# Kernel optimization log

Hardware: AMD Instinct MI355X
Metric: run time of the kernel (lower is better)

The kernel has to match this reference:

```python
import jax, jax.numpy as jnp
import numpy as np

NUM_HEADS = 16


def setup_inputs() -> dict:
    key = jax.random.key(0)
    ks = jax.random.split(key, 5)
    b, s, d = 2, 2048, 1024
    std = (2.0 / (d + d)) ** 0.5
    x = jax.random.normal(ks[0], (b, s, d), dtype=jnp.float32)
    Wq = jax.random.normal(ks[1], (d, d), dtype=jnp.float32) * std
    Wk = jax.random.normal(ks[2], (d, d), dtype=jnp.float32) * std
    Wv = jax.random.normal(ks[3], (d, d), dtype=jnp.float32) * std
    Wo = jax.random.normal(ks[4], (d, d), dtype=jnp.float32) * std
    return {"x": x, "Wq": Wq, "Wk": Wk, "Wv": Wv, "Wo": Wo}


def reference(x, Wq, Wk, Wv, Wo):
    b, s, d = x.shape
    h = NUM_HEADS
    dk = d // h
    # projections: bias-free x @ W (W is [in, out])
    def split_heads(t):
        return t.reshape(b, s, h, dk).transpose(0, 2, 1, 3)  # b h s dk
    q = split_heads(x @ Wq)
    k = split_heads(x @ Wk)
    v = split_heads(x @ Wv)
    scale = 1.0 / jnp.sqrt(jnp.asarray(dk, dtype=x.dtype))
    scores = jnp.einsum('bhqd,bhkd->bhqk', q, k) * scale  # b h s s
    causal = jnp.tril(jnp.ones((s, s), dtype=bool))
    scores = jnp.where(causal, scores, -jnp.inf)
    probs = jax.nn.softmax(scores, axis=-1)
    out = jnp.einsum('bhqk,bhkd->bhqd', probs, v)
    out = out.transpose(0, 2, 1, 3).reshape(b, s, d)  # b s (h dk)
    return out @ Wo
```

## Files before the change

### kernel.cpp

```cpp
#include <hip/hip_runtime.h>

typedef unsigned short u16;
typedef unsigned int   u32;

using bf16x8 = __attribute__((ext_vector_type(8))) __bf16;
using bf16x4 = __attribute__((ext_vector_type(4))) __bf16;
using f32x4  = __attribute__((ext_vector_type(4))) float;
using s16x4  = __attribute__((ext_vector_type(4))) short;

#define NH    16
#define DKH   64
#define SEQ   2048
#define BAT   2
#define DMOD  1024

#define QSCALE 0.18033688011112042f

__device__ __forceinline__ u16 f2bf(float f) {
  union { float f; u32 u; } v; v.f = f;
  u32 r = v.u + 0x7fffu + ((v.u >> 16) & 1u);
  return (u16)(r >> 16);
}

__device__ __forceinline__ u32 pack2bf(float a, float b) {
  union { float f; u32 u; } x, y; x.f = a; y.f = b;
  u32 ua = x.u + 0x7fffu + ((x.u >> 16) & 1u);
  u32 ub = y.u + 0x7fffu + ((y.u >> 16) & 1u);
  return __builtin_amdgcn_perm(ub, ua, 0x07060302u);
}

__device__ __forceinline__ s16x4 pk4bf(float a, float b, float c, float d) {
  union { bf16x4 bv; s16x4 sv; } u;
  u.bv[0] = (__bf16)a; u.bv[1] = (__bf16)b; u.bv[2] = (__bf16)c; u.bv[3] = (__bf16)d;
  return u.sv;
}

#if __has_builtin(__builtin_amdgcn_exp2f)
#define EXP2(x) __builtin_amdgcn_exp2f(x)
#else
#define EXP2(x) exp2f(x)
#endif

#if __has_builtin(__builtin_amdgcn_mfma_f32_16x16x16bf16_1k)
__device__ __forceinline__ f32x4 mfma16(s16x4 a, s16x4 b, f32x4 c) {
  return __builtin_amdgcn_mfma_f32_16x16x16bf16_1k(a, b, c, 0, 0, 0);
}
#else
__device__ __forceinline__ f32x4 mfma16(s16x4 a, s16x4 b, f32x4 c) {
  f32x4 d;
  asm volatile("v_mfma_f32_16x16x16_bf16 %0, %1, %2, %3\n\ts_nop 7\n\ts_nop 7"
               : "=v"(d) : "v"(a), "v"(b), "v"(c));
  return d;
}
#endif

__global__ __launch_bounds__(256) void transpose_all(const float* __restrict__ Wq,
                                                     const float* __restrict__ Wk,
                                                     const float* __restrict__ Wv,
                                                     const float* __restrict__ Wo,
                                                     u16* __restrict__ Wt) {
  __shared__ u16 t[32][33];
  const float* W = blockIdx.z == 0 ? Wq : blockIdx.z == 1 ? Wk : blockIdx.z == 2 ? Wv : Wo;
  u16* o = Wt + (size_t)blockIdx.z * DMOD * DMOD;
  int bx = blockIdx.x * 32, by = blockIdx.y * 32;
  int x = threadIdx.x, y = threadIdx.y;
  #pragma unroll
  for (int i = 0; i < 32; i += 8)
    t[y + i][x] = f2bf(W[(size_t)(by + y + i) * DMOD + bx + x]);
  __syncthreads();
  #pragma unroll
  for (int i = 0; i < 32; i += 8)
    o[(size_t)(bx + y + i) * DMOD + by + x] = t[x][y + i];
}

__global__ __launch_bounds__(256) void convert_x(const float* __restrict__ x,
                                                 u16* __restrict__ xb) {
  size_t i = ((size_t)blockIdx.x * 256 + threadIdx.x) * 8;
  float4 f0 = *(const float4*)(x + i);
  float4 f1 = *(const float4*)(x + i + 4);
  uint4 o;
  o.x = pack2bf(f0.x, f0.y); o.y = pack2bf(f0.z, f0.w);
  o.z = pack2bf(f1.x, f1.y); o.w = pack2bf(f1.z, f1.w);
  *(uint4*)(xb + i) = o;
}

__global__ __launch_bounds__(256, 3) void gemm_qkv(const u16* __restrict__ A,
                                                   const u16* __restrict__ Bt,
                                                   u16* __restrict__ Qo,
                                                   u16* __restrict__ Ko,
                                                   u16* __restrict__ Vo) {
  __shared__ __align__(16) u16 As[128 * 40];
  __shared__ __align__(16) u16 Bs[128 * 40];
  const int tid  = threadIdx.x;
  const int lane = tid & 63, wv = tid >> 6;
  const int wm   = wv >> 1, wn = wv & 1;
  const int lrow = lane & 15, quad = lane >> 4;
  const int tileM = blockIdx.x * 128, tileN = blockIdx.y * 128;
  const int r0 = tid >> 2, c0 = (tid & 3) * 8;
  const int r1 = r0 + 64;

  const f32x4 fz = {0.f, 0.f, 0.f, 0.f};
  f32x4 acc[4][4];
  #pragma unroll
  for (int i = 0; i < 4; ++i)
    #pragma unroll
    for (int j = 0; j < 4; ++j) acc[i][j] = fz;

  uint4 a0 = *(const uint4*)(&A [(size_t)(tileM + r0) * DMOD + c0]);
  uint4 a1 = *(const uint4*)(&A [(size_t)(tileM + r1) * DMOD + c0]);
  uint4 b0 = *(const uint4*)(&Bt[(size_t)(tileN + r0) * DMOD + c0]);
  uint4 b1 = *(const uint4*)(&Bt[(size_t)(tileN + r1) * DMOD + c0]);

  for (int kt = 0; kt < DMOD; kt += 32) {
    __syncthreads();
    *(uint4*)(&As[r0 * 40 + c0]) = a0;
    *(uint4*)(&As[r1 * 40 + c0]) = a1;
    *(uint4*)(&Bs[r0 * 40 + c0]) = b0;
    *(uint4*)(&Bs[r1 * 40 + c0]) = b1;
    if (kt + 32 < DMOD) {
      a0 = *(const uint4*)(&A [(size_t)(tileM + r0) * DMOD + kt + 32 + c0]);
      a1 = *(const uint4*)(&A [(size_t)(tileM + r1) * DMOD + kt + 32 + c0]);
      b0 = *(const uint4*)(&Bt[(size_t)(tileN + r0) * DMOD + kt + 32 + c0]);
      b1 = *(const uint4*)(&Bt[(size_t)(tileN + r1) * DMOD + kt + 32 + c0]);
    }
    __syncthreads();
    bf16x8 af[4], bfr[4];
    #pragma unroll
    for (int mt = 0; mt < 4; ++mt)
      af[mt] = *(const bf16x8*)(&As[(wm * 64 + mt * 16 + lrow) * 40 + quad * 8]);
    #pragma unroll
    for (int nt = 0; nt < 4; ++nt)
      bfr[nt] = *(const bf16x8*)(&Bs[(wn * 64 + nt * 16 + lrow) * 40 + quad * 8]);
    #pragma unroll
    for (int mt = 0; mt < 4; ++mt)
      #pragma unroll
      for (int nt = 0; nt < 4; ++nt)
        acc[mt][nt] = __builtin_amdgcn_mfma_f32_16x16x32_bf16(af[mt], bfr[nt],
                                                              acc[mt][nt], 0, 0, 0);
  }

  #pragma unroll
  for (int mt = 0; mt < 4; ++mt) {
    #pragma unroll
    for (int nt = 0; nt < 4; ++nt) {
      int gm0 = tileM + wm * 64 + mt * 16 + quad * 4;
      int gn  = tileN + wn * 64 + nt * 16 + lrow;
      int which = gn >> 10, col = gn & 1023;
      int bb = gm0 >> 11, srw0 = gm0 & (SEQ - 1);
      int hh = col >> 6, dki = col & (DKH - 1);
      size_t bhi = (size_t)(bb * NH + hh);
      if (which == 0) {
        #pragma unroll
        for (int r = 0; r < 4; ++r)
          Qo[(bhi * SEQ + srw0 + r) * DKH + dki] = f2bf(acc[mt][nt][r] * QSCALE);
      } else if (which == 1) {
        #pragma unroll
        for (int r = 0; r < 4; ++r)
          Ko[(bhi * SEQ + srw0 + r) * DKH + dki] = f2bf(acc[mt][nt][r]);
      } else {
        uint2 pk;
        pk.x = pack2bf(acc[mt][nt][0], acc[mt][nt][1]);
        pk.y = pack2bf(acc[mt][nt][2], acc[mt][nt][3]);
        *(uint2*)(&Vo[(((bhi * (SEQ / 4)) + (srw0 >> 2)) * DKH + dki) * 4]) = pk;
      }
    }
  }
}

__global__ __launch_bounds__(256, 3) void gemm_out(const u16* __restrict__ A,
                                                   const u16* __restrict__ Bt,
                                                   float* __restrict__ Co) {
  __shared__ __align__(16) u16 As[128 * 40];
  __shared__ __align__(16) u16 Bs[64 * 40];
  const int tid  = threadIdx.x;
  const int lane = tid & 63, wv = tid >> 6;
  const int wm   = wv & 1, wn = wv >> 1;
  const int lrow = lane & 15, quad = lane >> 4;
  const int tileM = blockIdx.x * 128, tileN = blockIdx.y * 64;
  const int r0 = tid >> 2, c0 = (tid & 3) * 8;
  const int r1 = r0 + 64;

  const f32x4 fz = {0.f, 0.f, 0.f, 0.f};
  f32x4 acc[4][2];
  #pragma unroll
  for (int i = 0; i < 4; ++i) { acc[i][0] = fz; acc[i][1] = fz; }

  uint4 a0 = *(const uint4*)(&A [(size_t)(tileM + r0) * DMOD + c0]);
  uint4 a1 = *(const uint4*)(&A [(size_t)(tileM + r1) * DMOD + c0]);
  uint4 b0 = *(const uint4*)(&Bt[(size_t)(tileN + (r0 & 63)) * DMOD + c0]);

  for (int kt = 0; kt < DMOD; kt += 32) {
    __syncthreads();
    *(uint4*)(&As[r0 * 40 + c0]) = a0;
    *(uint4*)(&As[r1 * 40 + c0]) = a1;
    if (r0 < 64) *(uint4*)(&Bs[r0 * 40 + c0]) = b0;
    if (kt + 32 < DMOD) {
      a0 = *(const uint4*)(&A [(size_t)(tileM + r0) * DMOD + kt + 32 + c0]);
      a1 = *(const uint4*)(&A [(size_t)(tileM + r1) * DMOD + kt + 32 + c0]);
      b0 = *(const uint4*)(&Bt[(size_t)(tileN + (r0 & 63)) * DMOD + kt + 32 + c0]);
    }
    __syncthreads();
    bf16x8 af[4], bfr[2];
    #pragma unroll
    for (int mt = 0; mt < 4; ++mt)
      af[mt] = *(const bf16x8*)(&As[(wm * 64 + mt * 16 + lrow) * 40 + quad * 8]);
    #pragma unroll
    for (int nt = 0; nt < 2; ++nt)
      bfr[nt] = *(const bf16x8*)(&Bs[(wn * 32 + nt * 16 + lrow) * 40 + quad * 8]);
    #pragma unroll
    for (int mt = 0; mt < 4; ++mt)
      #pragma unroll
      for (int nt = 0; nt < 2; ++nt)
        acc[mt][nt] = __builtin_amdgcn_mfma_f32_16x16x32_bf16(af[mt], bfr[nt],
                                                              acc[mt][nt], 0, 0, 0);
  }

  #pragma unroll
  for (int mt = 0; mt < 4; ++mt)
    #pragma unroll
    for (int nt = 0; nt < 2; ++nt)
      #pragma unroll
      for (int r = 0; r < 4; ++r) {
        int gm = tileM + wm * 64 + mt * 16 + quad * 4 + r;
        int gn = tileN + wn * 32 + nt * 16 + lrow;
        Co[(size_t)gm * DMOD + gn] = acc[mt][nt][r];
      }
}

#define KP 72
#define VP 132
#define OP 68

__global__ __launch_bounds__(128, 2) void attn_k(const u16* __restrict__ Q,
                                                 const u16* __restrict__ Kg,
                                                 const u16* __restrict__ Vg,
                                                 u16* __restrict__ Og) {
  __shared__ __align__(16) u16 Ks[128 * KP];
  __shared__ __align__(16) u16 Vs[64 * VP];

  const int tid  = threadIdx.x;
  const int lane = tid & 63, w = tid >> 6;
  const int lrow = lane & 15, quad = lane >> 4;
  const int bh = blockIdx.x;
  const int t  = blockIdx.y;
  const int qb = (t < 16) ? t : 47 - t;
  const int b = bh >> 4, h = bh & 15;
  const int jmax = qb >> 1;
  const int qoff = qb & 1;

  const u16* Qbh = Q  + (size_t)bh * SEQ * DKH;
  const u16* Kbh = Kg + (size_t)bh * SEQ * DKH;
  const u16* Vbh = Vg + (size_t)bh * SEQ * DKH;

  bf16x8 bq[2][2];
  #pragma unroll
  for (int s = 0; s < 2; ++s)
    #pragma unroll
    for (int kk = 0; kk < 2; ++kk)
      bq[s][kk] = *(const bf16x8*)(&Qbh[(size_t)(qb * 64 + (2 * w + s) * 16 + lrow) * DKH
                                        + kk * 32 + quad * 8]);

  uint4 kreg[8], vreg[8];
  #pragma unroll
  for (int k = 0; k < 8; ++k) {
    int ci = k * 128 + tid;
    kreg[k] = *(const uint4*)(&Kbh[(size_t)(ci >> 3) * DKH + (ci & 7) * 8]);
    vreg[k] = *(const uint4*)(&Vbh[(size_t)(ci >> 5) * 256 + (ci & 31) * 8]);
  }

  const f32x4 fz = {0.f, 0.f, 0.f, 0.f};
  f32x4 oacc[2][4];
  #pragma unroll
  for (int s = 0; s < 2; ++s)
    #pragma unroll
    for (int d = 0; d < 4; ++d) oacc[s][d] = fz;
  float lsum[2] = {0.f, 0.f};

  for (int j = 0; j <= jmax; ++j) {
    if (j) __syncthreads();

    #pragma unroll
    for (int k = 0; k < 8; ++k) {
      int ci = k * 128 + tid;
      *(uint4*)(&Ks[(ci >> 3) * KP + (ci & 7) * 8]) = kreg[k];
      int sq = ci >> 5, dkp = ci & 31;
      union { uint4 q; uint2 d[2]; } vv; vv.q = vreg[k];
      *(uint2*)(&Vs[(2 * dkp)     * VP + 4 * sq]) = vv.d[0];
      *(uint2*)(&Vs[(2 * dkp + 1) * VP + 4 * sq]) = vv.d[1];
    }

    if (j < jmax) {
      const int jn = j + 1;
      #pragma unroll
      for (int k = 0; k < 8; ++k) {
        int ci = k * 128 + tid;
        kreg[k] = *(const uint4*)(&Kbh[(size_t)(jn * 128 + (ci >> 3)) * DKH + (ci & 7) * 8]);
        vreg[k] = *(const uint4*)(&Vbh[(size_t)(jn * 32 + (ci >> 5)) * 256 + (ci & 31) * 8]);
      }
    }

    __syncthreads();

    if (j < jmax) {
      f32x4 sacc[2][8];
      #pragma unroll
      for (int s = 0; s < 2; ++s)
        #pragma unroll
        for (int m = 0; m < 8; ++m) sacc[s][m] = fz;
      #pragma unroll
      for (int kk = 0; kk < 2; ++kk)
        #pragma unroll
        for (int m = 0; m < 8; ++m) {
          bf16x8 ak = *(const bf16x8*)(&Ks[(m * 16 + lrow) * KP + kk * 32 + quad * 8]);
          sacc[0][m] = __builtin_amdgcn_mfma_f32_16x16x32_bf16(ak, bq[0][kk], sacc[0][m], 0, 0, 0);
          sacc[1][m] = __builtin_amdgcn_mfma_f32_16x16x32_bf16(ak, bq[1][kk], sacc[1][m], 0, 0, 0);
        }
      #pragma unroll
      for (int m = 0; m < 8; ++m) {
        float p00 = EXP2(sacc[0][m][0]), p01 = EXP2(sacc[0][m][1]);
        float p02 = EXP2(sacc[0][m][2]), p03 = EXP2(sacc[0][m][3]);
        float p10 = EXP2(sacc[1][m][0]), p11 = EXP2(sacc[1][m][1]);
        float p12 = EXP2(sacc[1][m][2]), p13 = EXP2(sacc[1][m][3]);
        lsum[0] += (p00 + p01) + (p02 + p03);
        lsum[1] += (p10 + p11) + (p12 + p13);
        s16x4 pk0 = pk4bf(p00, p01, p02, p03);
        s16x4 pk1 = pk4bf(p10, p11, p12, p13);
        #pragma unroll
        for (int d = 0; d < 4; ++d) {
          s16x4 av = *(const s16x4*)(&Vs[(d * 16 + lrow) * VP + m * 16 + quad * 4]);
          oacc[0][d] = mfma16(av, pk0, oacc[0][d]);
          oacc[1][d] = mfma16(av, pk1, oacc[1][d]);
        }
      }
    } else {
      #pragma unroll
      for (int s = 0; s < 2; ++s) {
        const int L = qoff * 4 + 2 * w + s;
        for (int m = 0; m < L; ++m) {
          f32x4 sv = fz;
          #pragma unroll
          for (int kk = 0; kk < 2; ++kk) {
            bf16x8 ak = *(const bf16x8*)(&Ks[(m * 16 + lrow) * KP + kk * 32 + quad * 8]);
            sv = __builtin_amdgcn_mfma_f32_16x16x32_bf16(ak, bq[s][kk], sv, 0, 0, 0);
          }
          float p0 = EXP2(sv[0]), p1 = EXP2(sv[1]), p2 = EXP2(sv[2]), p3 = EXP2(sv[3]);
          lsum[s] += (p0 + p1) + (p2 + p3);
          s16x4 pk = pk4bf(p0, p1, p2, p3);
          #pragma unroll
          for (int d = 0; d < 4; ++d) {
            s16x4 av = *(const s16x4*)(&Vs[(d * 16 + lrow) * VP + m * 16 + quad * 4]);
            oacc[s][d] = mfma16(av, pk, oacc[s][d]);
          }
        }
        {
          f32x4 sv = fz;
          #pragma unroll
          for (int kk = 0; kk < 2; ++kk) {
            bf16x8 ak = *(const bf16x8*)(&Ks[(L * 16 + lrow) * KP + kk * 32 + quad * 8]);
            sv = __builtin_amdgcn_mfma_f32_16x16x32_bf16(ak, bq[s][kk], sv, 0, 0, 0);
          }
          float p[4];
          #pragma unroll
          for (int r = 0; r < 4; ++r)
            p[r] = (quad * 4 + r > lrow) ? 0.f : EXP2(sv[r]);
          lsum[s] += (p[0] + p[1]) + (p[2] + p[3]);
          s16x4 pk = pk4bf(p[0], p[1], p[2], p[3]);
          #pragma unroll
          for (int d = 0; d < 4; ++d) {
            s16x4 av = *(const s16x4*)(&Vs[(d * 16 + lrow) * VP + L * 16 + quad * 4]);
            oacc[s][d] = mfma16(av, pk, oacc[s][d]);
          }
        }
      }
    }
  }

  float inv[2];
  #pragma unroll
  for (int s = 0; s < 2; ++s) {
    float ls = lsum[s];
    ls += __shfl_xor(ls, 16, 64);
    ls += __shfl_xor(ls, 32, 64);
    inv[s] = 1.f / ls;
  }

  __syncthreads();
  u16* Osr = Ks;
  #pragma unroll
  for (int s = 0; s < 2; ++s) {
    int row = (2 * w + s) * 16 + lrow;
    #pragma unroll
    for (int d = 0; d < 4; ++d) {
      uint2 pkk;
      pkk.x = pack2bf(oacc[s][d][0] * inv[s], oacc[s][d][1] * inv[s]);
      pkk.y = pack2bf(oacc[s][d][2] * inv[s], oacc[s][d][3] * inv[s]);
      *(uint2*)(&Osr[row * OP + d * 16 + quad * 4]) = pkk;
    }
  }
  __syncthreads();
  #pragma unroll
  for (int k = 0; k < 4; ++k) {
    int c = k * 128 + tid;
    int row = c >> 3, ch = c & 7;
    uint4 v = *(const uint4*)(&Osr[row * OP + ch * 8]);
    *(uint4*)(&Og[(size_t)(b * SEQ + qb * 64 + row) * DMOD + h * DKH + ch * 8]) = v;
  }
}

extern "C" void kernel_launch(void* const* d_in, const int* in_sizes, int n_in,
                              void* d_out, int out_size, void* d_ws, size_t ws_size,
                              hipStream_t stream) {
  const float* x  = (const float*)d_in[0];
  const float* Wq = (const float*)d_in[1];
  const float* Wk = (const float*)d_in[2];
  const float* Wv = (const float*)d_in[3];
  const float* Wo = (const float*)d_in[4];

  u16* ws = (u16*)d_ws;
  const size_t WSZ = (size_t)DMOD * DMOD;
  const size_t TSZ = (size_t)BAT * NH * SEQ * DKH;
  u16* Wt  = ws;
  u16* Wto = Wt + 3 * WSZ;
  u16* xb  = Wt + 4 * WSZ;
  u16* Qb  = xb + TSZ;
  u16* Kb  = Qb + TSZ;
  u16* Vb  = Kb + TSZ;
  u16* Ob  = xb;

  transpose_all<<<dim3(32, 32, 4), dim3(32, 8), 0, stream>>>(Wq, Wk, Wv, Wo, Wt);
  convert_x<<<dim3(2048), 256, 0, stream>>>(x, xb);

  gemm_qkv<<<dim3(32, 24), 256, 0, stream>>>(xb, Wt, Qb, Kb, Vb);

  attn_k<<<dim3(32, 32), 128, 0, stream>>>(Qb, Kb, Vb, Ob);

  gemm_out<<<dim3(32, 16), 256, 0, stream>>>(Ob, Wto, (float*)d_out);
}
```

Baseline: 195.1 us.

## Use direct global-to-LDS loads in GEMMs and double-buffer larger attention tiles

Result: faster. 181.1 us (-7.2%).

```diff
diff --git a/kernel.cpp b/kernel.cpp
--- a/kernel.cpp
+++ b/kernel.cpp
@@ -53,6 +53,12 @@
   return d;
 }
 #endif
+
+typedef const __attribute__((address_space(1))) u32 glb_u32;
+typedef __attribute__((address_space(3))) u32 lds_u32;
+__device__ __forceinline__ void gload16(const u16* g, u16* l) {
+  __builtin_amdgcn_global_load_lds((glb_u32*)(const void*)g, (lds_u32*)(void*)l, 16, 0, 0);
+}
 
 __global__ __launch_bounds__(256) void transpose_all(const float* __restrict__ Wq,
                                                      const float* __restrict__ Wk,
@@ -89,15 +95,13 @@
                                                    u16* __restrict__ Qo,
                                                    u16* __restrict__ Ko,
                                                    u16* __restrict__ Vo) {
-  __shared__ __align__(16) u16 As[128 * 40];
-  __shared__ __align__(16) u16 Bs[128 * 40];
+  __shared__ __align__(16) u16 As[128 * 32];
+  __shared__ __align__(16) u16 Bs[128 * 32];
   const int tid  = threadIdx.x;
   const int lane = tid & 63, wv = tid >> 6;
   const int wm   = wv >> 1, wn = wv & 1;
   const int lrow = lane & 15, quad = lane >> 4;
   const int tileM = blockIdx.x * 128, tileN = blockIdx.y * 128;
-  const int r0 = tid >> 2, c0 = (tid & 3) * 8;
-  const int r1 = r0 + 64;
 
   const f32x4 fz = {0.f, 0.f, 0.f, 0.f};
   f32x4 acc[4][4];
@@ -106,31 +110,23 @@
     #pragma unroll
     for (int j = 0; j < 4; ++j) acc[i][j] = fz;
 
-  uint4 a0 = *(const uint4*)(&A [(size_t)(tileM + r0) * DMOD + c0]);
-  uint4 a1 = *(const uint4*)(&A [(size_t)(tileM + r1) * DMOD + c0]);
-  uint4 b0 = *(const uint4*)(&Bt[(size_t)(tileN + r0) * DMOD + c0]);
-  uint4 b1 = *(const uint4*)(&Bt[(size_t)(tileN + r1) * DMOD + c0]);
-
   for (int kt = 0; kt < DMOD; kt += 32) {
+    if (kt) __syncthreads();
+    #pragma unroll
+    for (int i = 0; i < 2; ++i) {
+      int idx = i * 256 + tid;
+      gload16(&A [(size_t)(tileM + (idx >> 2)) * DMOD + kt + (idx & 3) * 8], &As[idx * 8]);
+      gload16(&Bt[(size_t)(tileN + (idx >> 2)) * DMOD + kt + (idx & 3) * 8], &Bs[idx * 8]);
+    }
     __syncthreads();
-    *(uint4*)(&As[r0 * 40 + c0]) = a0;
-    *(uint4*)(&As[r1 * 40 + c0]) = a1;
-    *(uint4*)(&Bs[r0 * 40 + c0]) = b0;
-    *(uint4*)(&Bs[r1 * 40 + c0]) = b1;
-    if (kt + 32 < DMOD) {
-      a0 = *(const uint4*)(&A [(size_t)(tileM + r0) * DMOD + kt + 32 + c0]);
-      a1 = *(const uint4*)(&A [(size_t)(tileM + r1) * DMOD + kt + 32 + c0]);
-      b0 = *(const uint4*)(&Bt[(size_t)(tileN + r0) * DMOD + kt + 32 + c0]);
-      b1 = *(const uint4*)(&Bt[(size_t)(tileN + r1) * DMOD + kt + 32 + c0]);
-    }
-    __syncthreads();
+
     bf16x8 af[4], bfr[4];
     #pragma unroll
     for (int mt = 0; mt < 4; ++mt)
-      af[mt] = *(const bf16x8*)(&As[(wm * 64 + mt * 16 + lrow) * 40 + quad * 8]);
+      af[mt] = *(const bf16x8*)(&As[(wm * 64 + mt * 16 + lrow) * 32 + quad * 8]);
     #pragma unroll
     for (int nt = 0; nt < 4; ++nt)
-      bfr[nt] = *(const bf16x8*)(&Bs[(wn * 64 + nt * 16 + lrow) * 40 + quad * 8]);
+      bfr[nt] = *(const bf16x8*)(&Bs[(wn * 64 + nt * 16 + lrow) * 32 + quad * 8]);
     #pragma unroll
     for (int mt = 0; mt < 4; ++mt)
       #pragma unroll
@@ -170,43 +166,36 @@
 __global__ __launch_bounds__(256, 3) void gemm_out(const u16* __restrict__ A,
                                                    const u16* __restrict__ Bt,
                                                    float* __restrict__ Co) {
-  __shared__ __align__(16) u16 As[128 * 40];
-  __shared__ __align__(16) u16 Bs[64 * 40];
+  __shared__ __align__(16) u16 As[128 * 32];
+  __shared__ __align__(16) u16 Bs[64 * 32];
   const int tid  = threadIdx.x;
   const int lane = tid & 63, wv = tid >> 6;
   const int wm   = wv & 1, wn = wv >> 1;
   const int lrow = lane & 15, quad = lane >> 4;
   const int tileM = blockIdx.x * 128, tileN = blockIdx.y * 64;
-  const int r0 = tid >> 2, c0 = (tid & 3) * 8;
-  const int r1 = r0 + 64;
 
   const f32x4 fz = {0.f, 0.f, 0.f, 0.f};
   f32x4 acc[4][2];
   #pragma unroll
   for (int i = 0; i < 4; ++i) { acc[i][0] = fz; acc[i][1] = fz; }
 
-  uint4 a0 = *(const uint4*)(&A [(size_t)(tileM + r0) * DMOD + c0]);
-  uint4 a1 = *(const uint4*)(&A [(size_t)(tileM + r1) * DMOD + c0]);
-  uint4 b0 = *(const uint4*)(&Bt[(size_t)(tileN + (r0 & 63)) * DMOD + c0]);
-
   for (int kt = 0; kt < DMOD; kt += 32) {
+    if (kt) __syncthreads();
+    #pragma unroll
+    for (int i = 0; i < 2; ++i) {
+      int idx = i * 256 + tid;
+      gload16(&A[(size_t)(tileM + (idx >> 2)) * DMOD + kt + (idx & 3) * 8], &As[idx * 8]);
+    }
+    gload16(&Bt[(size_t)(tileN + (tid >> 2)) * DMOD + kt + (tid & 3) * 8], &Bs[tid * 8]);
     __syncthreads();
-    *(uint4*)(&As[r0 * 40 + c0]) = a0;
-    *(uint4*)(&As[r1 * 40 + c0]) = a1;
-    if (r0 < 64) *(uint4*)(&Bs[r0 * 40 + c0]) = b0;
-    if (kt + 32 < DMOD) {
-      a0 = *(const uint4*)(&A [(size_t)(tileM + r0) * DMOD + kt + 32 + c0]);
-      a1 = *(const uint4*)(&A [(size_t)(tileM + r1) * DMOD + kt + 32 + c0]);
-      b0 = *(const uint4*)(&Bt[(size_t)(tileN + (r0 & 63)) * DMOD + kt + 32 + c0]);
-    }
-    __syncthreads();
+
     bf16x8 af[4], bfr[2];
     #pragma unroll
     for (int mt = 0; mt < 4; ++mt)
-      af[mt] = *(const bf16x8*)(&As[(wm * 64 + mt * 16 + lrow) * 40 + quad * 8]);
+      af[mt] = *(const bf16x8*)(&As[(wm * 64 + mt * 16 + lrow) * 32 + quad * 8]);
     #pragma unroll
     for (int nt = 0; nt < 2; ++nt)
-      bfr[nt] = *(const bf16x8*)(&Bs[(wn * 32 + nt * 16 + lrow) * 40 + quad * 8]);
+      bfr[nt] = *(const bf16x8*)(&Bs[(wn * 32 + nt * 16 + lrow) * 32 + quad * 8]);
     #pragma unroll
     for (int mt = 0; mt < 4; ++mt)
       #pragma unroll
@@ -231,39 +220,41 @@
 #define VP 132
 #define OP 68
 
-__global__ __launch_bounds__(128, 2) void attn_k(const u16* __restrict__ Q,
+__global__ __launch_bounds__(256, 2) void attn_k(const u16* __restrict__ Q,
                                                  const u16* __restrict__ Kg,
                                                  const u16* __restrict__ Vg,
                                                  u16* __restrict__ Og) {
-  __shared__ __align__(16) u16 Ks[128 * KP];
-  __shared__ __align__(16) u16 Vs[64 * VP];
+  __shared__ __align__(16) u16 KsA[128 * KP];
+  __shared__ __align__(16) u16 VsA[64 * VP];
+  __shared__ __align__(16) u16 KsB[128 * KP];
+  __shared__ __align__(16) u16 VsB[64 * VP];
 
   const int tid  = threadIdx.x;
   const int lane = tid & 63, w = tid >> 6;
   const int lrow = lane & 15, quad = lane >> 4;
   const int bh = blockIdx.x;
   const int t  = blockIdx.y;
-  const int qb = (t < 16) ? t : 47 - t;
+  const int qt = (t < 8) ? t : 23 - t;
   const int b = bh >> 4, h = bh & 15;
-  const int jmax = qb >> 1;
-  const int qoff = qb & 1;
 
   const u16* Qbh = Q  + (size_t)bh * SEQ * DKH;
   const u16* Kbh = Kg + (size_t)bh * SEQ * DKH;
   const u16* Vbh = Vg + (size_t)bh * SEQ * DKH;
 
+  const int jmax = qt;
+
   bf16x8 bq[2][2];
   #pragma unroll
   for (int s = 0; s < 2; ++s)
     #pragma unroll
     for (int kk = 0; kk < 2; ++kk)
-      bq[s][kk] = *(const bf16x8*)(&Qbh[(size_t)(qb * 64 + (2 * w + s) * 16 + lrow) * DKH
+      bq[s][kk] = *(const bf16x8*)(&Qbh[(size_t)(qt * 128 + (2 * w + s) * 16 + lrow) * DKH
                                         + kk * 32 + quad * 8]);
 
-  uint4 kreg[8], vreg[8];
-  #pragma unroll
-  for (int k = 0; k < 8; ++k) {
-    int ci = k * 128 + tid;
+  uint4 kreg[4], vreg[4];
+  #pragma unroll
+  for (int k = 0; k < 4; ++k) {
+    int ci = k * 256 + tid;
     kreg[k] = *(const uint4*)(&Kbh[(size_t)(ci >> 3) * DKH + (ci & 7) * 8]);
     vreg[k] = *(const uint4*)(&Vbh[(size_t)(ci >> 5) * 256 + (ci & 31) * 8]);
   }
@@ -276,12 +267,14 @@
     for (int d = 0; d < 4; ++d) oacc[s][d] = fz;
   float lsum[2] = {0.f, 0.f};
 
+  int cur = 0;
   for (int j = 0; j <= jmax; ++j) {
-    if (j) __syncthreads();
-
-    #pragma unroll
-    for (int k = 0; k < 8; ++k) {
-      int ci = k * 128 + tid;
+    u16* Ks = cur ? KsB : KsA;
+    u16* Vs = cur ? VsB : VsA;
+
+    #pragma unroll
+    for (int k = 0; k < 4; ++k) {
+      int ci = k * 256 + tid;
       *(uint4*)(&Ks[(ci >> 3) * KP + (ci & 7) * 8]) = kreg[k];
       int sq = ci >> 5, dkp = ci & 31;
       union { uint4 q; uint2 d[2]; } vv; vv.q = vreg[k];
@@ -292,8 +285,8 @@
     if (j < jmax) {
       const int jn = j + 1;
       #pragma unroll
-      for (int k = 0; k < 8; ++k) {
-        int ci = k * 128 + tid;
+      for (int k = 0; k < 4; ++k) {
+        int ci = k * 256 + tid;
         kreg[k] = *(const uint4*)(&Kbh[(size_t)(jn * 128 + (ci >> 3)) * DKH + (ci & 7) * 8]);
         vreg[k] = *(const uint4*)(&Vbh[(size_t)(jn * 32 + (ci >> 5)) * 256 + (ci & 31) * 8]);
       }
@@ -302,6 +295,7 @@
     __syncthreads();
 
     if (j < jmax) {
+      __builtin_amdgcn_s_setprio(1);
       f32x4 sacc[2][8];
       #pragma unroll
       for (int s = 0; s < 2; ++s)
@@ -332,11 +326,12 @@
           oacc[1][d] = mfma16(av, pk1, oacc[1][d]);
         }
       }
+      __builtin_amdgcn_s_setprio(0);
     } else {
       #pragma unroll
       for (int s = 0; s < 2; ++s) {
-        const int L = qoff * 4 + 2 * w + s;
-        for (int m = 0; m < L; ++m) {
+        const int ss = 2 * w + s;
+        for (int m = 0; m < ss; ++m) {
           f32x4 sv = fz;
           #pragma unroll
           for (int kk = 0; kk < 2; ++kk) {
@@ -356,7 +351,7 @@
           f32x4 sv = fz;
           #pragma unroll
           for (int kk = 0; kk < 2; ++kk) {
-            bf16x8 ak = *(const bf16x8*)(&Ks[(L * 16 + lrow) * KP + kk * 32 + quad * 8]);
+            bf16x8 ak = *(const bf16x8*)(&Ks[(ss * 16 + lrow) * KP + kk * 32 + quad * 8]);
             sv = __builtin_amdgcn_mfma_f32_16x16x32_bf16(ak, bq[s][kk], sv, 0, 0, 0);
           }
           float p[4];
@@ -367,25 +362,26 @@
           s16x4 pk = pk4bf(p[0], p[1], p[2], p[3]);
           #pragma unroll
           for (int d = 0; d < 4; ++d) {
-            s16x4 av = *(const s16x4*)(&Vs[(d * 16 + lrow) * VP + L * 16 + quad * 4]);
+            s16x4 av = *(const s16x4*)(&Vs[(d * 16 + lrow) * VP + ss * 16 + quad * 4]);
             oacc[s][d] = mfma16(av, pk, oacc[s][d]);
           }
         }
       }
     }
+    cur ^= 1;
   }
 
   float inv[2];
   #pragma unroll
   for (int s = 0; s < 2; ++s) {
-    float ls = lsum[s];
-    ls += __shfl_xor(ls, 16, 64);
-    ls += __shfl_xor(ls, 32, 64);
-    inv[s] = 1.f / ls;
+    float v = lsum[s];
+    v += __shfl_xor(v, 16, 64);
+    v += __shfl_xor(v, 32, 64);
+    inv[s] = 1.f / v;
   }
 
   __syncthreads();
-  u16* Osr = Ks;
+  u16* Osr = KsA;
   #pragma unroll
   for (int s = 0; s < 2; ++s) {
     int row = (2 * w + s) * 16 + lrow;
@@ -400,10 +396,10 @@
   __syncthreads();
   #pragma unroll
   for (int k = 0; k < 4; ++k) {
-    int c = k * 128 + tid;
+    int c = k * 256 + tid;
     int row = c >> 3, ch = c & 7;
     uint4 v = *(const uint4*)(&Osr[row * OP + ch * 8]);
-    *(uint4*)(&Og[(size_t)(b * SEQ + qb * 64 + row) * DMOD + h * DKH + ch * 8]) = v;
+    *(uint4*)(&Og[(size_t)(b * SEQ + qt * 128 + row) * DMOD + h * DKH + ch * 8]) = v;
   }
 }
 
@@ -432,7 +428,7 @@
 
   gemm_qkv<<<dim3(32, 24), 256, 0, stream>>>(xb, Wt, Qb, Kb, Vb);
 
-  attn_k<<<dim3(32, 32), 128, 0, stream>>>(Qb, Kb, Vb, Ob);
+  attn_k<<<dim3(32, 16), 256, 0, stream>>>(Qb, Kb, Vb, Ob);
 
   gemm_out<<<dim3(32, 16), 256, 0, stream>>>(Ob, Wto, (float*)d_out);
 }
```
